# Kernel optimization log

Hardware: AMD Instinct MI355X
Metric: run time of the kernel (lower is better)

## Reference

```python
import jax, jax.numpy as jnp
import numpy as np

D_MODEL = 1024
NUM_HEADS = 16
D_K = D_MODEL // NUM_HEADS
SCALE = float(np.sqrt(D_K))


def setup_inputs() -> dict:
    key = jax.random.key(0)
    ks = jax.random.split(key, 6)
    x = jax.random.normal(ks[0], (2, 2048, D_MODEL), dtype=jnp.float32)
    s = 1.0 / np.sqrt(D_MODEL)
    w_q = jax.random.uniform(ks[1], (D_MODEL, D_MODEL), jnp.float32, -s, s)
    w_k = jax.random.uniform(ks[2], (D_MODEL, D_MODEL), jnp.float32, -s, s)
    w_v = jax.random.uniform(ks[3], (D_MODEL, D_MODEL), jnp.float32, -s, s)
    w_o = jax.random.uniform(ks[4], (D_MODEL, D_MODEL), jnp.float32, -s, s)
    b_o = jax.random.uniform(ks[5], (D_MODEL,), jnp.float32, -s, s)
    return {"x": x, "w_q": w_q, "w_k": w_k, "w_v": w_v, "w_o": w_o, "b_o": b_o}


def reference(x, w_q, w_k, w_v, w_o, b_o):
    B, S, _ = x.shape
    # project and split heads: [B, H, S, d_k]
    def heads(w):
        return (x @ w.T).reshape(B, S, NUM_HEADS, D_K).transpose(0, 2, 1, 3)
    Q, K, V = heads(w_q), heads(w_k), heads(w_v)
    scores = jnp.einsum("bhqd,bhkd->bhqk", Q, K) / SCALE  # [B,H,S,S]
    attn = jax.nn.softmax(scores, axis=-1)
    context = jnp.einsum("bhqk,bhkd->bhqd", attn, V)
    context = context.transpose(0, 2, 1, 3).reshape(B, S, D_MODEL)
    return context @ w_o.T + b_o
```

## Files before the change

kernel.cpp:

```cpp
#include <hip/hip_runtime.h>

typedef unsigned short u16t;
typedef short bf16x8 __attribute__((ext_vector_type(8)));
typedef short bf16x4 __attribute__((ext_vector_type(4)));
typedef float f32x4 __attribute__((ext_vector_type(4)));

#define NHEADS 16
#define SEQ 2048
#define DMODEL 1024
#define HEAD_ELEMS (SEQ * 64)
#define LSTR 72
#define MATE ((size_t)2 * SEQ * DMODEL)
#define CSC 0.1803368801f
#define MB 4.0f

__device__ __forceinline__ u16t f2bf(float f) {
  union { float f; unsigned u; } v; v.f = f;
  unsigned r = v.u + 0x7FFFu + ((v.u >> 16) & 1u);
  return (u16t)(r >> 16);
}
__device__ __forceinline__ float bf2f(u16t b) {
  union { unsigned u; float f; } v; v.u = ((unsigned)b) << 16;
  return v.f;
}
__device__ __forceinline__ float sanef(float x) {
  return fminf(fmaxf(x, -16384.f), 16384.f);
}
__device__ __forceinline__ unsigned pk2(float a, float b) {
  union { float f; unsigned u; } x, y; x.f = a; y.f = b;
  return __builtin_amdgcn_perm(y.u + 0x8000u, x.u + 0x8000u, 0x07060302u);
}
__device__ __forceinline__ bf16x8 cvt8(const float* p) {
  const f32x4* q4 = (const f32x4*)p;
  f32x4 a = q4[0], b = q4[1];
  bf16x8 o;
  o[0] = (short)f2bf(a[0]); o[1] = (short)f2bf(a[1]);
  o[2] = (short)f2bf(a[2]); o[3] = (short)f2bf(a[3]);
  o[4] = (short)f2bf(b[0]); o[5] = (short)f2bf(b[1]);
  o[6] = (short)f2bf(b[2]); o[7] = (short)f2bf(b[3]);
  return o;
}

__device__ __forceinline__ void stage16(const u16t* g, u16t* l) {
  __builtin_amdgcn_global_load_lds(
      (const __attribute__((address_space(1))) unsigned int*)g,
      (__attribute__((address_space(3))) unsigned int*)l, 16, 0, 0);
}

struct ushort4a { u16t x, y, z, w; } __attribute__((aligned(8)));

__device__ __forceinline__ int detect_bf16_wave(const u16t* p) {
  int lane = threadIdx.x & 63;
  int cnt = 0;
#pragma unroll
  for (int i = 0; i < 8; ++i) {
    int ex = (p[2 * (lane * 8 + i)] >> 7) & 0xFF;
    cnt += (ex >= 100 && ex <= 140) ? 1 : 0;
  }
  cnt += __shfl_xor(cnt, 1);
  cnt += __shfl_xor(cnt, 2);
  cnt += __shfl_xor(cnt, 4);
  cnt += __shfl_xor(cnt, 8);
  cnt += __shfl_xor(cnt, 16);
  cnt += __shfl_xor(cnt, 32);
  return cnt >= 300;
}

__global__ __launch_bounds__(256) void qkv_kernel(
    const void* __restrict__ xv,
    const void* __restrict__ wqv, const void* __restrict__ wkv,
    const void* __restrict__ wvv,
    u16t* __restrict__ q_ws, u16t* __restrict__ k_ws, u16t* __restrict__ vt_ws) {
  __shared__ u16t As[128 * 32];
  __shared__ u16t Bs[128 * 32];
  const int bfm = detect_bf16_wave((const u16t*)xv);
  const int tid = threadIdx.x;
  const int bm0 = blockIdx.x * 128;
  const int bn0 = blockIdx.y * 128;
  const int z = blockIdx.z;
  const void* Wv = (z == 0) ? wqv : ((z == 1) ? wkv : wvv);
  const float scale = (z == 0) ? CSC : 1.0f;
  const int lane = tid & 63;
  const int w = tid >> 6;
  const int ln = lane & 15;
  const int quad = lane >> 4;
  const int wm = (w & 1) * 64;
  const int wn = (w >> 1) * 64;

  f32x4 acc[4][4] = {};

  for (int kt = 0; kt < 32; ++kt) {
    __syncthreads();
    if (bfm) {
      const u16t* x = (const u16t*)xv;
      const u16t* W = (const u16t*)Wv;
#pragma unroll
      for (int j = 0; j < 2; ++j) {
        int f = j * 256 + tid;
        int row = f >> 2;
        int col = (f & 3) * 8;
        stage16(x + (size_t)(bm0 + row) * DMODEL + kt * 32 + col, &As[f * 8]);
        stage16(W + (size_t)(bn0 + row) * DMODEL + kt * 32 + col, &Bs[f * 8]);
      }
    } else {
      const float* x = (const float*)xv;
      const float* W = (const float*)Wv;
#pragma unroll
      for (int j = 0; j < 2; ++j) {
        int f = j * 256 + tid;
        int row = f >> 2;
        int col = (f & 3) * 8;
        bf16x8 ra = cvt8(x + (size_t)(bm0 + row) * DMODEL + kt * 32 + col);
        bf16x8 rb = cvt8(W + (size_t)(bn0 + row) * DMODEL + kt * 32 + col);
        *(bf16x8*)&As[f * 8] = ra;
        *(bf16x8*)&Bs[f * 8] = rb;
      }
    }
    __syncthreads();
    bf16x8 a[4], b[4];
#pragma unroll
    for (int t = 0; t < 4; ++t)
      a[t] = *(const bf16x8*)&As[(wm + t * 16 + ln) * 32 + quad * 8];
#pragma unroll
    for (int t = 0; t < 4; ++t)
      b[t] = *(const bf16x8*)&Bs[(wn + t * 16 + ln) * 32 + quad * 8];
#pragma unroll
    for (int i = 0; i < 4; ++i)
#pragma unroll
      for (int jn = 0; jn < 4; ++jn)
        acc[i][jn] = __builtin_amdgcn_mfma_f32_16x16x32_bf16(a[i], b[jn], acc[i][jn], 0, 0, 0);
  }

#pragma unroll
  for (int i = 0; i < 4; ++i) {
    int m_base = bm0 + wm + i * 16 + quad * 4;
#pragma unroll
    for (int jn = 0; jn < 4; ++jn) {
      int n = bn0 + wn + jn * 16 + ln;
      int h = n >> 6, dk = n & 63;
      if (z < 2) {
        u16t* dst = (z == 0) ? q_ws : k_ws;
#pragma unroll
        for (int r = 0; r < 4; ++r) {
          int m = m_base + r;
          int bb = m >> 11, s = m & 2047;
          dst[(size_t)(bb * NHEADS + h) * HEAD_ELEMS + s * 64 + dk] =
              f2bf(sanef(acc[i][jn][r]) * scale);
        }
      } else {
        int bb = m_base >> 11, s = m_base & 2047;
        ushort4a pk;
        pk.x = f2bf(sanef(acc[i][jn][0]));
        pk.y = f2bf(sanef(acc[i][jn][1]));
        pk.z = f2bf(sanef(acc[i][jn][2]));
        pk.w = f2bf(sanef(acc[i][jn][3]));
        *(ushort4a*)&vt_ws[(size_t)(bb * NHEADS + h) * HEAD_ELEMS + (size_t)dk * SEQ + s] = pk;
      }
    }
  }
}

__global__ __launch_bounds__(512, 4) void attn_kernel(
    const u16t* __restrict__ q_ws, const u16t* __restrict__ k_ws,
    const u16t* __restrict__ vt_ws, u16t* __restrict__ ctx_ws) {
  __shared__ u16t Ks[64 * LSTR];
  __shared__ u16t Vt[64 * LSTR];
  const int tid = threadIdx.x;
  const int w = tid >> 6;
  const int lane = tid & 63;
  const int ln = lane & 15;
  const int quad = lane >> 4;
  const int bh = blockIdx.y;
  const size_t base = (size_t)bh * HEAD_ELEMS;
  const int q0w = blockIdx.x * 128 + w * 16;

  bf16x8 aq[2];
#pragma unroll
  for (int ks = 0; ks < 2; ++ks)
    aq[ks] = *(const bf16x8*)(q_ws + base + (size_t)(q0w + ln) * 64 + ks * 32 + quad * 8);

  const int r = tid >> 3;
  const int cc = (tid & 7) * 8;
  const u16t* kp = k_ws + base + (size_t)tid * 8;
  const u16t* vp = vt_ws + base + (size_t)r * SEQ + cc;
  u16t* kl = &Ks[r * LSTR + cc];
  u16t* vl = &Vt[r * LSTR + cc];

  f32x4 accO[4] = {};
  float psum = 0.f;

  for (int kt = 0; kt < 32; ++kt) {
    bf16x8 rk = *(const bf16x8*)kp; kp += 4096;
    bf16x8 rv = *(const bf16x8*)vp; vp += 64;
    __syncthreads();
    *(bf16x8*)kl = rk;
    *(bf16x8*)vl = rv;
    __syncthreads();

    f32x4 st[4];
#pragma unroll
    for (int nt = 0; nt < 4; ++nt) {
      st[nt][0] = -MB; st[nt][1] = -MB; st[nt][2] = -MB; st[nt][3] = -MB;
    }
#pragma unroll
    for (int nt = 0; nt < 4; ++nt)
#pragma unroll
      for (int ks = 0; ks < 2; ++ks) {
        bf16x8 bk = *(const bf16x8*)&Ks[(nt * 16 + ln) * LSTR + ks * 32 + quad * 8];
        st[nt] = __builtin_amdgcn_mfma_f32_16x16x32_bf16(bk, aq[ks], st[nt], 0, 0, 0);
      }

#pragma unroll
    for (int pp = 0; pp < 2; ++pp) {
      float pv[8];
#pragma unroll
      for (int j = 0; j < 4; ++j) {
        pv[j]     = exp2f(st[2 * pp][j]);
        pv[4 + j] = exp2f(st[2 * pp + 1][j]);
      }
      psum += ((pv[0] + pv[1]) + (pv[2] + pv[3])) + ((pv[4] + pv[5]) + (pv[6] + pv[7]));
      union { unsigned u[4]; bf16x8 v; } ap;
      ap.u[0] = pk2(pv[0], pv[1]);
      ap.u[1] = pk2(pv[2], pv[3]);
      ap.u[2] = pk2(pv[4], pv[5]);
      ap.u[3] = pk2(pv[6], pv[7]);
#pragma unroll
      for (int dt = 0; dt < 4; ++dt) {
        const u16t* vrow = &Vt[(dt * 16 + ln) * LSTR + quad * 4];
        bf16x4 lo = *(const bf16x4*)(vrow + (2 * pp) * 16);
        bf16x4 hi = *(const bf16x4*)(vrow + (2 * pp + 1) * 16);
        bf16x8 bb = __builtin_shufflevector(lo, hi, 0, 1, 2, 3, 4, 5, 6, 7);
        accO[dt] = __builtin_amdgcn_mfma_f32_16x16x32_bf16(ap.v, bb, accO[dt], 0, 0, 0);
      }
    }
  }

  psum += __shfl_xor(psum, 16);
  psum += __shfl_xor(psum, 32);
  float inv[4];
#pragma unroll
  for (int rr = 0; rr < 4; ++rr) {
    float lq = __shfl(psum, quad * 4 + rr);
    inv[rr] = 1.0f / fmaxf(lq, 1e-20f);
  }
#pragma unroll
  for (int dt = 0; dt < 4; ++dt)
#pragma unroll
    for (int rr = 0; rr < 4; ++rr)
      ctx_ws[base + (size_t)(q0w + quad * 4 + rr) * 64 + dt * 16 + ln] =
          f2bf(accO[dt][rr] * inv[rr]);
}

__global__ __launch_bounds__(256) void outproj_kernel(
    const u16t* __restrict__ ctx, const void* __restrict__ wov,
    const void* __restrict__ bov_, void* __restrict__ outv) {
  __shared__ u16t As[128 * 32];
  __shared__ u16t Bs[128 * 32];
  const int bfm = detect_bf16_wave((const u16t*)wov);
  const int tid = threadIdx.x;
  const int bm0 = blockIdx.x * 128;
  const int bn0 = blockIdx.y * 128;
  const int lane = tid & 63;
  const int w = tid >> 6;
  const int ln = lane & 15;
  const int quad = lane >> 4;
  const int wm = (w & 1) * 64;
  const int wn = (w >> 1) * 64;

  f32x4 acc[4][4] = {};

  for (int kt = 0; kt < 32; ++kt) {
    __syncthreads();
#pragma unroll
    for (int j = 0; j < 2; ++j) {
      int f = j * 256 + tid;
      int row = f >> 2;
      int col = (f & 3) * 8;
      int m = bm0 + row;
      int bb = m >> 11, s = m & 2047;
      int k = kt * 32 + col;
      int h = k >> 6, dk = k & 63;
      stage16(ctx + (size_t)(bb * NHEADS + h) * HEAD_ELEMS + s * 64 + dk, &As[f * 8]);
      if (bfm) {
        stage16((const u16t*)wov + (size_t)(bn0 + row) * DMODEL + kt * 32 + col, &Bs[f * 8]);
      } else {
        bf16x8 rb = cvt8((const float*)wov + (size_t)(bn0 + row) * DMODEL + kt * 32 + col);
        *(bf16x8*)&Bs[f * 8] = rb;
      }
    }
    __syncthreads();
    bf16x8 a[4], b[4];
#pragma unroll
    for (int t = 0; t < 4; ++t)
      a[t] = *(const bf16x8*)&As[(wm + t * 16 + ln) * 32 + quad * 8];
#pragma unroll
    for (int t = 0; t < 4; ++t)
      b[t] = *(const bf16x8*)&Bs[(wn + t * 16 + ln) * 32 + quad * 8];
#pragma unroll
    for (int i = 0; i < 4; ++i)
#pragma unroll
      for (int jn = 0; jn < 4; ++jn)
        acc[i][jn] = __builtin_amdgcn_mfma_f32_16x16x32_bf16(a[i], b[jn], acc[i][jn], 0, 0, 0);
  }

#pragma unroll
  for (int i = 0; i < 4; ++i) {
    int m_base = bm0 + wm + i * 16 + quad * 4;
#pragma unroll
    for (int jn = 0; jn < 4; ++jn) {
      int n = bn0 + wn + jn * 16 + ln;
      float bov = bfm ? bf2f(((const u16t*)bov_)[n]) : ((const float*)bov_)[n];
#pragma unroll
      for (int r = 0; r < 4; ++r) {
        int m = m_base + r;
        float v = sanef(acc[i][jn][r] + bov);
        if (bfm) ((u16t*)outv)[(size_t)m * DMODEL + n] = f2bf(v);
        else     ((float*)outv)[(size_t)m * DMODEL + n] = v;
      }
    }
  }
}

extern "C" void kernel_launch(void* const* d_in, const int* in_sizes, int n_in,
                              void* d_out, int out_size, void* d_ws, size_t ws_size,
                              hipStream_t stream) {
  (void)in_sizes; (void)n_in; (void)out_size; (void)ws_size;
  const void* x  = d_in[0];
  const void* wq = d_in[1];
  const void* wk = d_in[2];
  const void* wv = d_in[3];
  const void* wo = d_in[4];
  const void* bo = d_in[5];

  u16t* q_ws  = (u16t*)d_ws;
  u16t* k_ws  = q_ws + MATE;
  u16t* vt_ws = k_ws + MATE;
  u16t* ctx_ws = q_ws;

  dim3 gA(32, 8, 3);
  qkv_kernel<<<gA, 256, 0, stream>>>(x, wq, wk, wv, q_ws, k_ws, vt_ws);

  dim3 gB(16, 32);
  attn_kernel<<<gB, 512, 0, stream>>>(q_ws, k_ws, vt_ws, ctx_ws);

  dim3 gC(32, 8);
  outproj_kernel<<<gC, 256, 0, stream>>>(ctx_ws, wo, bo, d_out);
}
```

Before: 233.4 us.

## Double-buffer LDS tiles in attention and GEMMs, retile out-projection, vectorize stores

```diff
diff --git a/kernel.cpp b/kernel.cpp
--- a/kernel.cpp
+++ b/kernel.cpp
@@ -10,6 +10,7 @@
 #define DMODEL 1024
 #define HEAD_ELEMS (SEQ * 64)
 #define LSTR 72
+#define QSTR 40
 #define MATE ((size_t)2 * SEQ * DMODEL)
 #define CSC 0.1803368801f
 #define MB 4.0f
@@ -41,12 +42,6 @@
   return o;
 }
 
-__device__ __forceinline__ void stage16(const u16t* g, u16t* l) {
-  __builtin_amdgcn_global_load_lds(
-      (const __attribute__((address_space(1))) unsigned int*)g,
-      (__attribute__((address_space(3))) unsigned int*)l, 16, 0, 0);
-}
-
 struct ushort4a { u16t x, y, z, w; } __attribute__((aligned(8)));
 
 __device__ __forceinline__ int detect_bf16_wave(const u16t* p) {
@@ -66,13 +61,13 @@
   return cnt >= 300;
 }
 
-__global__ __launch_bounds__(256) void qkv_kernel(
+__global__ __launch_bounds__(256, 3) void qkv_kernel(
     const void* __restrict__ xv,
     const void* __restrict__ wqv, const void* __restrict__ wkv,
     const void* __restrict__ wvv,
     u16t* __restrict__ q_ws, u16t* __restrict__ k_ws, u16t* __restrict__ vt_ws) {
-  __shared__ u16t As[128 * 32];
-  __shared__ u16t Bs[128 * 32];
+  __shared__ u16t As[2][128 * QSTR];
+  __shared__ u16t Bs[2][128 * QSTR];
   const int bfm = detect_bf16_wave((const u16t*)xv);
   const int tid = threadIdx.x;
   const int bm0 = blockIdx.x * 128;
@@ -89,72 +84,111 @@
 
   f32x4 acc[4][4] = {};
 
-  for (int kt = 0; kt < 32; ++kt) {
+  auto do_mfma = [&](int cur) {
+    bf16x8 a[4], b[4];
+#pragma unroll
+    for (int t = 0; t < 4; ++t)
+      a[t] = *(const bf16x8*)&As[cur][(wm + t * 16 + ln) * QSTR + quad * 8];
+#pragma unroll
+    for (int t = 0; t < 4; ++t)
+      b[t] = *(const bf16x8*)&Bs[cur][(wn + t * 16 + ln) * QSTR + quad * 8];
+    if (z < 2) {
+#pragma unroll
+      for (int p = 0; p < 4; ++p)
+#pragma unroll
+        for (int q = 0; q < 4; ++q)
+          acc[p][q] = __builtin_amdgcn_mfma_f32_16x16x32_bf16(b[p], a[q], acc[p][q], 0, 0, 0);
+    } else {
+#pragma unroll
+      for (int p = 0; p < 4; ++p)
+#pragma unroll
+        for (int q = 0; q < 4; ++q)
+          acc[p][q] = __builtin_amdgcn_mfma_f32_16x16x32_bf16(a[p], b[q], acc[p][q], 0, 0, 0);
+    }
+  };
+
+  if (bfm) {
+    const u16t* x = (const u16t*)xv;
+    const u16t* W = (const u16t*)Wv;
+    const int c0 = tid, c1 = tid + 256;
+    const int r0 = c0 >> 2, o0 = (c0 & 3) * 8;
+    const int r1 = c1 >> 2, o1 = (c1 & 3) * 8;
+    const u16t* xa0 = x + (size_t)(bm0 + r0) * DMODEL + o0;
+    const u16t* xa1 = x + (size_t)(bm0 + r1) * DMODEL + o1;
+    const u16t* wb0 = W + (size_t)(bn0 + r0) * DMODEL + o0;
+    const u16t* wb1 = W + (size_t)(bn0 + r1) * DMODEL + o1;
+    const int d0 = r0 * QSTR + o0, d1 = r1 * QSTR + o1;
+
+    bf16x8 ra0 = *(const bf16x8*)xa0, ra1 = *(const bf16x8*)xa1;
+    bf16x8 rb0 = *(const bf16x8*)wb0, rb1 = *(const bf16x8*)wb1;
+    *(bf16x8*)&As[0][d0] = ra0; *(bf16x8*)&As[0][d1] = ra1;
+    *(bf16x8*)&Bs[0][d0] = rb0; *(bf16x8*)&Bs[0][d1] = rb1;
     __syncthreads();
-    if (bfm) {
-      const u16t* x = (const u16t*)xv;
-      const u16t* W = (const u16t*)Wv;
+    for (int kt = 0; kt < 32; ++kt) {
+      int cur = kt & 1;
+      if (kt < 31) {
+        xa0 += 32; xa1 += 32; wb0 += 32; wb1 += 32;
+        ra0 = *(const bf16x8*)xa0; ra1 = *(const bf16x8*)xa1;
+        rb0 = *(const bf16x8*)wb0; rb1 = *(const bf16x8*)wb1;
+      }
+      do_mfma(cur);
+      if (kt < 31) {
+        int nxt = cur ^ 1;
+        *(bf16x8*)&As[nxt][d0] = ra0; *(bf16x8*)&As[nxt][d1] = ra1;
+        *(bf16x8*)&Bs[nxt][d0] = rb0; *(bf16x8*)&Bs[nxt][d1] = rb1;
+        __syncthreads();
+      }
+    }
+  } else {
+    const float* x = (const float*)xv;
+    const float* W = (const float*)Wv;
+    for (int kt = 0; kt < 32; ++kt) {
+      __syncthreads();
 #pragma unroll
       for (int j = 0; j < 2; ++j) {
-        int f = j * 256 + tid;
-        int row = f >> 2;
-        int col = (f & 3) * 8;
-        stage16(x + (size_t)(bm0 + row) * DMODEL + kt * 32 + col, &As[f * 8]);
-        stage16(W + (size_t)(bn0 + row) * DMODEL + kt * 32 + col, &Bs[f * 8]);
-      }
-    } else {
-      const float* x = (const float*)xv;
-      const float* W = (const float*)Wv;
-#pragma unroll
-      for (int j = 0; j < 2; ++j) {
-        int f = j * 256 + tid;
-        int row = f >> 2;
-        int col = (f & 3) * 8;
-        bf16x8 ra = cvt8(x + (size_t)(bm0 + row) * DMODEL + kt * 32 + col);
-        bf16x8 rb = cvt8(W + (size_t)(bn0 + row) * DMODEL + kt * 32 + col);
-        *(bf16x8*)&As[f * 8] = ra;
-        *(bf16x8*)&Bs[f * 8] = rb;
-      }
-    }
-    __syncthreads();
-    bf16x8 a[4], b[4];
-#pragma unroll
-    for (int t = 0; t < 4; ++t)
-      a[t] = *(const bf16x8*)&As[(wm + t * 16 + ln) * 32 + quad * 8];
-#pragma unroll
-    for (int t = 0; t < 4; ++t)
-      b[t] = *(const bf16x8*)&Bs[(wn + t * 16 + ln) * 32 + quad * 8];
-#pragma unroll
-    for (int i = 0; i < 4; ++i)
-#pragma unroll
-      for (int jn = 0; jn < 4; ++jn)
-        acc[i][jn] = __builtin_amdgcn_mfma_f32_16x16x32_bf16(a[i], b[jn], acc[i][jn], 0, 0, 0);
-  }
-
-#pragma unroll
-  for (int i = 0; i < 4; ++i) {
-    int m_base = bm0 + wm + i * 16 + quad * 4;
-#pragma unroll
-    for (int jn = 0; jn < 4; ++jn) {
-      int n = bn0 + wn + jn * 16 + ln;
-      int h = n >> 6, dk = n & 63;
-      if (z < 2) {
-        u16t* dst = (z == 0) ? q_ws : k_ws;
-#pragma unroll
-        for (int r = 0; r < 4; ++r) {
-          int m = m_base + r;
-          int bb = m >> 11, s = m & 2047;
-          dst[(size_t)(bb * NHEADS + h) * HEAD_ELEMS + s * 64 + dk] =
-              f2bf(sanef(acc[i][jn][r]) * scale);
-        }
-      } else {
-        int bb = m_base >> 11, s = m_base & 2047;
+        int c = j * 256 + tid;
+        int row = c >> 2, col = (c & 3) * 8;
+        *(bf16x8*)&As[0][row * QSTR + col] = cvt8(x + (size_t)(bm0 + row) * DMODEL + kt * 32 + col);
+        *(bf16x8*)&Bs[0][row * QSTR + col] = cvt8(W + (size_t)(bn0 + row) * DMODEL + kt * 32 + col);
+      }
+      __syncthreads();
+      do_mfma(0);
+    }
+  }
+
+  if (z < 2) {
+    u16t* dst = (z == 0) ? q_ws : k_ws;
+#pragma unroll
+    for (int p = 0; p < 4; ++p) {
+      int n_base = bn0 + wn + p * 16 + quad * 4;
+      int h = n_base >> 6, dkb = n_base & 63;
+#pragma unroll
+      for (int q = 0; q < 4; ++q) {
+        int m = bm0 + wm + q * 16 + ln;
+        int bb = m >> 11, sq = m & 2047;
         ushort4a pk;
-        pk.x = f2bf(sanef(acc[i][jn][0]));
-        pk.y = f2bf(sanef(acc[i][jn][1]));
-        pk.z = f2bf(sanef(acc[i][jn][2]));
-        pk.w = f2bf(sanef(acc[i][jn][3]));
-        *(ushort4a*)&vt_ws[(size_t)(bb * NHEADS + h) * HEAD_ELEMS + (size_t)dk * SEQ + s] = pk;
+        pk.x = f2bf(sanef(acc[p][q][0]) * scale);
+        pk.y = f2bf(sanef(acc[p][q][1]) * scale);
+        pk.z = f2bf(sanef(acc[p][q][2]) * scale);
+        pk.w = f2bf(sanef(acc[p][q][3]) * scale);
+        *(ushort4a*)&dst[(size_t)(bb * NHEADS + h) * HEAD_ELEMS + sq * 64 + dkb] = pk;
+      }
+    }
+  } else {
+#pragma unroll
+    for (int p = 0; p < 4; ++p) {
+      int m_base = bm0 + wm + p * 16 + quad * 4;
+      int bb = m_base >> 11, sq = m_base & 2047;
+#pragma unroll
+      for (int q = 0; q < 4; ++q) {
+        int n = bn0 + wn + q * 16 + ln;
+        int h = n >> 6, dk = n & 63;
+        ushort4a pk;
+        pk.x = f2bf(sanef(acc[p][q][0]));
+        pk.y = f2bf(sanef(acc[p][q][1]));
+        pk.z = f2bf(sanef(acc[p][q][2]));
+        pk.w = f2bf(sanef(acc[p][q][3]));
+        *(ushort4a*)&vt_ws[(size_t)(bb * NHEADS + h) * HEAD_ELEMS + (size_t)dk * SEQ + sq] = pk;
       }
     }
   }
@@ -163,8 +197,8 @@
 __global__ __launch_bounds__(512, 4) void attn_kernel(
     const u16t* __restrict__ q_ws, const u16t* __restrict__ k_ws,
     const u16t* __restrict__ vt_ws, u16t* __restrict__ ctx_ws) {
-  __shared__ u16t Ks[64 * LSTR];
-  __shared__ u16t Vt[64 * LSTR];
+  __shared__ u16t Ks[2][64 * LSTR];
+  __shared__ u16t Vt[2][64 * LSTR];
   const int tid = threadIdx.x;
   const int w = tid >> 6;
   const int lane = tid & 63;
@@ -181,21 +215,26 @@
 
   const int r = tid >> 3;
   const int cc = (tid & 7) * 8;
+  const int d = r * LSTR + cc;
   const u16t* kp = k_ws + base + (size_t)tid * 8;
   const u16t* vp = vt_ws + base + (size_t)r * SEQ + cc;
-  u16t* kl = &Ks[r * LSTR + cc];
-  u16t* vl = &Vt[r * LSTR + cc];
 
   f32x4 accO[4] = {};
   float psum = 0.f;
 
+  bf16x8 rk = *(const bf16x8*)kp;
+  bf16x8 rv = *(const bf16x8*)vp;
+  *(bf16x8*)&Ks[0][d] = rk;
+  *(bf16x8*)&Vt[0][d] = rv;
+  __syncthreads();
+
   for (int kt = 0; kt < 32; ++kt) {
-    bf16x8 rk = *(const bf16x8*)kp; kp += 4096;
-    bf16x8 rv = *(const bf16x8*)vp; vp += 64;
-    __syncthreads();
-    *(bf16x8*)kl = rk;
-    *(bf16x8*)vl = rv;
-    __syncthreads();
+    const int cur = kt & 1;
+    if (kt < 31) {
+      kp += 4096; vp += 64;
+      rk = *(const bf16x8*)kp;
+      rv = *(const bf16x8*)vp;
+    }
 
     f32x4 st[4];
 #pragma unroll
@@ -206,7 +245,7 @@
     for (int nt = 0; nt < 4; ++nt)
 #pragma unroll
       for (int ks = 0; ks < 2; ++ks) {
-        bf16x8 bk = *(const bf16x8*)&Ks[(nt * 16 + ln) * LSTR + ks * 32 + quad * 8];
+        bf16x8 bk = *(const bf16x8*)&Ks[cur][(nt * 16 + ln) * LSTR + ks * 32 + quad * 8];
         st[nt] = __builtin_amdgcn_mfma_f32_16x16x32_bf16(bk, aq[ks], st[nt], 0, 0, 0);
       }
 
@@ -226,13 +265,20 @@
       ap.u[3] = pk2(pv[6], pv[7]);
 #pragma unroll
       for (int dt = 0; dt < 4; ++dt) {
-        const u16t* vrow = &Vt[(dt * 16 + ln) * LSTR + quad * 4];
+        const u16t* vrow = &Vt[cur][(dt * 16 + ln) * LSTR + quad * 4];
         bf16x4 lo = *(const bf16x4*)(vrow + (2 * pp) * 16);
         bf16x4 hi = *(const bf16x4*)(vrow + (2 * pp + 1) * 16);
         bf16x8 bb = __builtin_shufflevector(lo, hi, 0, 1, 2, 3, 4, 5, 6, 7);
         accO[dt] = __builtin_amdgcn_mfma_f32_16x16x32_bf16(ap.v, bb, accO[dt], 0, 0, 0);
       }
     }
+
+    if (kt < 31) {
+      const int nxt = cur ^ 1;
+      *(bf16x8*)&Ks[nxt][d] = rk;
+      *(bf16x8*)&Vt[nxt][d] = rv;
+      __syncthreads();
+    }
   }
 
   psum += __shfl_xor(psum, 16);
@@ -251,71 +297,112 @@
           f2bf(accO[dt][rr] * inv[rr]);
 }
 
-__global__ __launch_bounds__(256) void outproj_kernel(
+__global__ __launch_bounds__(256, 4) void outproj_kernel(
     const u16t* __restrict__ ctx, const void* __restrict__ wov,
     const void* __restrict__ bov_, void* __restrict__ outv) {
-  __shared__ u16t As[128 * 32];
-  __shared__ u16t Bs[128 * 32];
+  __shared__ u16t As[2][64 * LSTR];
+  __shared__ u16t Bs[2][64 * LSTR];
   const int bfm = detect_bf16_wave((const u16t*)wov);
   const int tid = threadIdx.x;
-  const int bm0 = blockIdx.x * 128;
-  const int bn0 = blockIdx.y * 128;
+  const int bm0 = blockIdx.x * 64;
+  const int bn0 = blockIdx.y * 64;
   const int lane = tid & 63;
   const int w = tid >> 6;
   const int ln = lane & 15;
   const int quad = lane >> 4;
-  const int wm = (w & 1) * 64;
-  const int wn = (w >> 1) * 64;
-
-  f32x4 acc[4][4] = {};
-
-  for (int kt = 0; kt < 32; ++kt) {
+  const int wm = (w & 1) * 32;
+  const int wn = (w >> 1) * 32;
+
+  f32x4 acc[2][2] = {};
+
+  auto do_mfma = [&](int cur) {
+    bf16x8 a[2][2], b[2][2];
+#pragma unroll
+    for (int t = 0; t < 2; ++t)
+#pragma unroll
+      for (int ks = 0; ks < 2; ++ks) {
+        a[t][ks] = *(const bf16x8*)&As[cur][(wm + t * 16 + ln) * LSTR + ks * 32 + quad * 8];
+        b[t][ks] = *(const bf16x8*)&Bs[cur][(wn + t * 16 + ln) * LSTR + ks * 32 + quad * 8];
+      }
+#pragma unroll
+    for (int p = 0; p < 2; ++p)
+#pragma unroll
+      for (int q = 0; q < 2; ++q)
+#pragma unroll
+        for (int ks = 0; ks < 2; ++ks)
+          acc[p][q] = __builtin_amdgcn_mfma_f32_16x16x32_bf16(b[p][ks], a[q][ks], acc[p][q], 0, 0, 0);
+  };
+
+  const int c0 = tid, c1 = tid + 256;
+  const int r0 = c0 >> 3, o0 = (c0 & 7) * 8;
+  const int r1 = c1 >> 3, o1 = (c1 & 7) * 8;
+  const int d0 = r0 * LSTR + o0, d1 = r1 * LSTR + o1;
+  const int m0 = bm0 + r0, m1 = bm0 + r1;
+  const u16t* ap0 = ctx + (size_t)((m0 >> 11) * NHEADS) * HEAD_ELEMS + (m0 & 2047) * 64 + o0;
+  const u16t* ap1 = ctx + (size_t)((m1 >> 11) * NHEADS) * HEAD_ELEMS + (m1 & 2047) * 64 + o1;
+
+  if (bfm) {
+    const u16t* wo = (const u16t*)wov;
+    const u16t* bp0 = wo + (size_t)(bn0 + r0) * DMODEL + o0;
+    const u16t* bp1 = wo + (size_t)(bn0 + r1) * DMODEL + o1;
+    bf16x8 ra0 = *(const bf16x8*)ap0, ra1 = *(const bf16x8*)ap1;
+    bf16x8 rb0 = *(const bf16x8*)bp0, rb1 = *(const bf16x8*)bp1;
+    *(bf16x8*)&As[0][d0] = ra0; *(bf16x8*)&As[0][d1] = ra1;
+    *(bf16x8*)&Bs[0][d0] = rb0; *(bf16x8*)&Bs[0][d1] = rb1;
     __syncthreads();
-#pragma unroll
-    for (int j = 0; j < 2; ++j) {
-      int f = j * 256 + tid;
-      int row = f >> 2;
-      int col = (f & 3) * 8;
-      int m = bm0 + row;
-      int bb = m >> 11, s = m & 2047;
-      int k = kt * 32 + col;
-      int h = k >> 6, dk = k & 63;
-      stage16(ctx + (size_t)(bb * NHEADS + h) * HEAD_ELEMS + s * 64 + dk, &As[f * 8]);
+    for (int kt = 0; kt < 16; ++kt) {
+      int cur = kt & 1;
+      if (kt < 15) {
+        ap0 += HEAD_ELEMS; ap1 += HEAD_ELEMS;
+        bp0 += 64; bp1 += 64;
+        ra0 = *(const bf16x8*)ap0; ra1 = *(const bf16x8*)ap1;
+        rb0 = *(const bf16x8*)bp0; rb1 = *(const bf16x8*)bp1;
+      }
+      do_mfma(cur);
+      if (kt < 15) {
+        int nxt = cur ^ 1;
+        *(bf16x8*)&As[nxt][d0] = ra0; *(bf16x8*)&As[nxt][d1] = ra1;
+        *(bf16x8*)&Bs[nxt][d0] = rb0; *(bf16x8*)&Bs[nxt][d1] = rb1;
+        __syncthreads();
+      }
+    }
+  } else {
+    const float* wo = (const float*)wov;
+    for (int kt = 0; kt < 16; ++kt) {
+      __syncthreads();
+      *(bf16x8*)&As[0][d0] = *(const bf16x8*)(ap0 + (size_t)kt * HEAD_ELEMS);
+      *(bf16x8*)&As[0][d1] = *(const bf16x8*)(ap1 + (size_t)kt * HEAD_ELEMS);
+      *(bf16x8*)&Bs[0][d0] = cvt8(wo + (size_t)(bn0 + r0) * DMODEL + kt * 64 + o0);
+      *(bf16x8*)&Bs[0][d1] = cvt8(wo + (size_t)(bn0 + r1) * DMODEL + kt * 64 + o1);
+      __syncthreads();
+      do_mfma(0);
+    }
+  }
+
+#pragma unroll
+  for (int p = 0; p < 2; ++p) {
+    int n_base = bn0 + wn + p * 16 + quad * 4;
+    float bv0, bv1, bv2, bv3;
+    if (bfm) {
+      ushort4a bb = *(const ushort4a*)&((const u16t*)bov_)[n_base];
+      bv0 = bf2f(bb.x); bv1 = bf2f(bb.y); bv2 = bf2f(bb.z); bv3 = bf2f(bb.w);
+    } else {
+      const float* bf = (const float*)bov_;
+      bv0 = bf[n_base]; bv1 = bf[n_base + 1]; bv2 = bf[n_base + 2]; bv3 = bf[n_base + 3];
+    }
+#pragma unroll
+    for (int q = 0; q < 2; ++q) {
+      int m = bm0 + wm + q * 16 + ln;
+      float v0 = sanef(acc[p][q][0]) + bv0;
+      float v1 = sanef(acc[p][q][1]) + bv1;
+      float v2 = sanef(acc[p][q][2]) + bv2;
+      float v3 = sanef(acc[p][q][3]) + bv3;
       if (bfm) {
-        stage16((const u16t*)wov + (size_t)(bn0 + row) * DMODEL + kt * 32 + col, &Bs[f * 8]);
+        ushort4a pk; pk.x = f2bf(v0); pk.y = f2bf(v1); pk.z = f2bf(v2); pk.w = f2bf(v3);
+        *(ushort4a*)&((u16t*)outv)[(size_t)m * DMODEL + n_base] = pk;
       } else {
-        bf16x8 rb = cvt8((const float*)wov + (size_t)(bn0 + row) * DMODEL + kt * 32 + col);
-        *(bf16x8*)&Bs[f * 8] = rb;
-      }
-    }
-    __syncthreads();
-    bf16x8 a[4], b[4];
-#pragma unroll
-    for (int t = 0; t < 4; ++t)
-      a[t] = *(const bf16x8*)&As[(wm + t * 16 + ln) * 32 + quad * 8];
-#pragma unroll
-    for (int t = 0; t < 4; ++t)
-      b[t] = *(const bf16x8*)&Bs[(wn + t * 16 + ln) * 32 + quad * 8];
-#pragma unroll
-    for (int i = 0; i < 4; ++i)
-#pragma unroll
-      for (int jn = 0; jn < 4; ++jn)
-        acc[i][jn] = __builtin_amdgcn_mfma_f32_16x16x32_bf16(a[i], b[jn], acc[i][jn], 0, 0, 0);
-  }
-
-#pragma unroll
-  for (int i = 0; i < 4; ++i) {
-    int m_base = bm0 + wm + i * 16 + quad * 4;
-#pragma unroll
-    for (int jn = 0; jn < 4; ++jn) {
-      int n = bn0 + wn + jn * 16 + ln;
-      float bov = bfm ? bf2f(((const u16t*)bov_)[n]) : ((const float*)bov_)[n];
-#pragma unroll
-      for (int r = 0; r < 4; ++r) {
-        int m = m_base + r;
-        float v = sanef(acc[i][jn][r] + bov);
-        if (bfm) ((u16t*)outv)[(size_t)m * DMODEL + n] = f2bf(v);
-        else     ((float*)outv)[(size_t)m * DMODEL + n] = v;
+        f32x4 pk; pk[0] = v0; pk[1] = v1; pk[2] = v2; pk[3] = v3;
+        *(f32x4*)&((float*)outv)[(size_t)m * DMODEL + n_base] = pk;
       }
     }
   }
@@ -343,6 +430,6 @@
   dim3 gB(16, 32);
   attn_kernel<<<gB, 512, 0, stream>>>(q_ws, k_ws, vt_ws, ctx_ws);
 
-  dim3 gC(32, 8);
+  dim3 gC(64, 16);
   outproj_kernel<<<gC, 256, 0, stream>>>(ctx_ws, wo, bo, d_out);
 }
```

New measurement: 234.7 us. About the same (+0.6%).

## Shrink out-projection tiles to 64x64 with padded LDS and double buffering

Applied to the files above, without the earlier changes.

```diff
diff --git a/kernel.cpp b/kernel.cpp
--- a/kernel.cpp
+++ b/kernel.cpp
@@ -110,10 +110,8 @@
         int f = j * 256 + tid;
         int row = f >> 2;
         int col = (f & 3) * 8;
-        bf16x8 ra = cvt8(x + (size_t)(bm0 + row) * DMODEL + kt * 32 + col);
-        bf16x8 rb = cvt8(W + (size_t)(bn0 + row) * DMODEL + kt * 32 + col);
-        *(bf16x8*)&As[f * 8] = ra;
-        *(bf16x8*)&Bs[f * 8] = rb;
+        *(bf16x8*)&As[f * 8] = cvt8(x + (size_t)(bm0 + row) * DMODEL + kt * 32 + col);
+        *(bf16x8*)&Bs[f * 8] = cvt8(W + (size_t)(bn0 + row) * DMODEL + kt * 32 + col);
       }
     }
     __syncthreads();
@@ -251,69 +249,99 @@
           f2bf(accO[dt][rr] * inv[rr]);
 }
 
-__global__ __launch_bounds__(256) void outproj_kernel(
+__global__ __launch_bounds__(256, 4) void outproj_kernel(
     const u16t* __restrict__ ctx, const void* __restrict__ wov,
     const void* __restrict__ bov_, void* __restrict__ outv) {
-  __shared__ u16t As[128 * 32];
-  __shared__ u16t Bs[128 * 32];
+  __shared__ u16t As[2][64 * LSTR];
+  __shared__ u16t Bs[2][64 * LSTR];
   const int bfm = detect_bf16_wave((const u16t*)wov);
   const int tid = threadIdx.x;
-  const int bm0 = blockIdx.x * 128;
-  const int bn0 = blockIdx.y * 128;
+  const int bm0 = blockIdx.x * 64;
+  const int bn0 = blockIdx.y * 64;
   const int lane = tid & 63;
   const int w = tid >> 6;
   const int ln = lane & 15;
   const int quad = lane >> 4;
-  const int wm = (w & 1) * 64;
-  const int wn = (w >> 1) * 64;
-
-  f32x4 acc[4][4] = {};
-
-  for (int kt = 0; kt < 32; ++kt) {
-    __syncthreads();
-#pragma unroll
-    for (int j = 0; j < 2; ++j) {
-      int f = j * 256 + tid;
-      int row = f >> 2;
-      int col = (f & 3) * 8;
-      int m = bm0 + row;
-      int bb = m >> 11, s = m & 2047;
-      int k = kt * 32 + col;
-      int h = k >> 6, dk = k & 63;
-      stage16(ctx + (size_t)(bb * NHEADS + h) * HEAD_ELEMS + s * 64 + dk, &As[f * 8]);
-      if (bfm) {
-        stage16((const u16t*)wov + (size_t)(bn0 + row) * DMODEL + kt * 32 + col, &Bs[f * 8]);
-      } else {
-        bf16x8 rb = cvt8((const float*)wov + (size_t)(bn0 + row) * DMODEL + kt * 32 + col);
-        *(bf16x8*)&Bs[f * 8] = rb;
-      }
-    }
-    __syncthreads();
-    bf16x8 a[4], b[4];
-#pragma unroll
-    for (int t = 0; t < 4; ++t)
-      a[t] = *(const bf16x8*)&As[(wm + t * 16 + ln) * 32 + quad * 8];
-#pragma unroll
-    for (int t = 0; t < 4; ++t)
-      b[t] = *(const bf16x8*)&Bs[(wn + t * 16 + ln) * 32 + quad * 8];
-#pragma unroll
-    for (int i = 0; i < 4; ++i)
-#pragma unroll
-      for (int jn = 0; jn < 4; ++jn)
-        acc[i][jn] = __builtin_amdgcn_mfma_f32_16x16x32_bf16(a[i], b[jn], acc[i][jn], 0, 0, 0);
-  }
-
-#pragma unroll
-  for (int i = 0; i < 4; ++i) {
-    int m_base = bm0 + wm + i * 16 + quad * 4;
-#pragma unroll
-    for (int jn = 0; jn < 4; ++jn) {
-      int n = bn0 + wn + jn * 16 + ln;
+  const int wm = (w & 1) * 32;
+  const int wn = (w >> 1) * 32;
+
+  f32x4 acc[2][2] = {};
+
+  auto do_mfma = [&](int cur) {
+    bf16x8 a[2][2], b[2][2];
+#pragma unroll
+    for (int t = 0; t < 2; ++t)
+#pragma unroll
+      for (int ks = 0; ks < 2; ++ks) {
+        a[t][ks] = *(const bf16x8*)&As[cur][(wm + t * 16 + ln) * LSTR + ks * 32 + quad * 8];
+        b[t][ks] = *(const bf16x8*)&Bs[cur][(wn + t * 16 + ln) * LSTR + ks * 32 + quad * 8];
+      }
+#pragma unroll
+    for (int p = 0; p < 2; ++p)
+#pragma unroll
+      for (int q = 0; q < 2; ++q)
+#pragma unroll
+        for (int ks = 0; ks < 2; ++ks)
+          acc[p][q] = __builtin_amdgcn_mfma_f32_16x16x32_bf16(a[p][ks], b[q][ks], acc[p][q], 0, 0, 0);
+  };
+
+  const int c0 = tid, c1 = tid + 256;
+  const int r0 = c0 >> 3, o0 = (c0 & 7) * 8;
+  const int r1 = c1 >> 3, o1 = (c1 & 7) * 8;
+  const int d0 = r0 * LSTR + o0, d1 = r1 * LSTR + o1;
+  const int m0 = bm0 + r0, m1 = bm0 + r1;
+  const u16t* ap0 = ctx + (size_t)((m0 >> 11) * NHEADS) * HEAD_ELEMS + (m0 & 2047) * 64 + o0;
+  const u16t* ap1 = ctx + (size_t)((m1 >> 11) * NHEADS) * HEAD_ELEMS + (m1 & 2047) * 64 + o1;
+
+  if (bfm) {
+    const u16t* wo = (const u16t*)wov;
+    const u16t* bp0 = wo + (size_t)(bn0 + r0) * DMODEL + o0;
+    const u16t* bp1 = wo + (size_t)(bn0 + r1) * DMODEL + o1;
+    bf16x8 ra0 = *(const bf16x8*)ap0, ra1 = *(const bf16x8*)ap1;
+    bf16x8 rb0 = *(const bf16x8*)bp0, rb1 = *(const bf16x8*)bp1;
+    *(bf16x8*)&As[0][d0] = ra0; *(bf16x8*)&As[0][d1] = ra1;
+    *(bf16x8*)&Bs[0][d0] = rb0; *(bf16x8*)&Bs[0][d1] = rb1;
+    __syncthreads();
+    for (int kt = 0; kt < 16; ++kt) {
+      int cur = kt & 1;
+      if (kt < 15) {
+        ap0 += HEAD_ELEMS; ap1 += HEAD_ELEMS;
+        bp0 += 64; bp1 += 64;
+        ra0 = *(const bf16x8*)ap0; ra1 = *(const bf16x8*)ap1;
+        rb0 = *(const bf16x8*)bp0; rb1 = *(const bf16x8*)bp1;
+      }
+      do_mfma(cur);
+      if (kt < 15) {
+        int nxt = cur ^ 1;
+        *(bf16x8*)&As[nxt][d0] = ra0; *(bf16x8*)&As[nxt][d1] = ra1;
+        *(bf16x8*)&Bs[nxt][d0] = rb0; *(bf16x8*)&Bs[nxt][d1] = rb1;
+        __syncthreads();
+      }
+    }
+  } else {
+    const float* wo = (const float*)wov;
+    for (int kt = 0; kt < 16; ++kt) {
+      __syncthreads();
+      *(bf16x8*)&As[0][d0] = *(const bf16x8*)(ap0 + (size_t)kt * HEAD_ELEMS);
+      *(bf16x8*)&As[0][d1] = *(const bf16x8*)(ap1 + (size_t)kt * HEAD_ELEMS);
+      *(bf16x8*)&Bs[0][d0] = cvt8(wo + (size_t)(bn0 + r0) * DMODEL + kt * 64 + o0);
+      *(bf16x8*)&Bs[0][d1] = cvt8(wo + (size_t)(bn0 + r1) * DMODEL + kt * 64 + o1);
+      __syncthreads();
+      do_mfma(0);
+    }
+  }
+
+#pragma unroll
+  for (int p = 0; p < 2; ++p) {
+    int m_base = bm0 + wm + p * 16 + quad * 4;
+#pragma unroll
+    for (int q = 0; q < 2; ++q) {
+      int n = bn0 + wn + q * 16 + ln;
       float bov = bfm ? bf2f(((const u16t*)bov_)[n]) : ((const float*)bov_)[n];
 #pragma unroll
-      for (int r = 0; r < 4; ++r) {
+      for (int r = 0; r < 2 * 2; ++r) {
         int m = m_base + r;
-        float v = sanef(acc[i][jn][r] + bov);
+        float v = sanef(acc[p][q][r] + bov);
         if (bfm) ((u16t*)outv)[(size_t)m * DMODEL + n] = f2bf(v);
         else     ((float*)outv)[(size_t)m * DMODEL + n] = v;
       }
@@ -343,6 +371,6 @@
   dim3 gB(16, 32);
   attn_kernel<<<gB, 512, 0, stream>>>(q_ws, k_ws, vt_ws, ctx_ws);
 
-  dim3 gC(32, 8);
+  dim3 gC(64, 16);
   outproj_kernel<<<gC, 256, 0, stream>>>(ctx_ws, wo, bo, d_out);
 }
```

Result: faster. 216.5 us (-7.2%).
